# Kernel tuning notes

Measured on AMD Instinct MI355X. Metric: run time of the kernel, lower is better.

## Reference

```python
import jax, jax.numpy as jnp
import numpy as np

B, T, S = 32, 64, 64
V, E, H, Hs = 32000, 512, 512, 512
D2 = 2 * Hs  # src feature dim


def setup_inputs() -> dict:
    key = jax.random.key(0)
    ks = jax.random.split(key, 26)
    n = lambda k, shape, s=0.05: (jax.random.normal(k, shape, jnp.float32) * s)
    inp = {
        'src': jax.random.normal(ks[0], (B, S, D2), jnp.float32),
        'trg': jax.random.randint(ks[1], (B, T), 0, V),
        'mask': jnp.ones((B, T), jnp.float32),
        'emb': n(ks[2], (V, E)),
        # PyTorch LSTMCell params: weight_ih [4H, E+H], weight_hh [4H, H]
        'f_Wih': n(ks[3], (4 * H, E + H)), 'f_Whh': n(ks[4], (4 * H, H)),
        'f_bih': n(ks[5], (4 * H,)), 'f_bhh': n(ks[6], (4 * H,)),
        'b_Wih': n(ks[7], (4 * H, E + H)), 'b_Whh': n(ks[8], (4 * H, H)),
        'b_bih': n(ks[9], (4 * H,)), 'b_bhh': n(ks[10], (4 * H,)),
        # attention projections: hidden -> 2*src_hidden
        'fatt_W': n(ks[11], (D2, H)), 'fatt_b': n(ks[12], (D2,)),
        'batt_W': n(ks[13], (D2, H)), 'batt_b': n(ks[14], (D2,)),
        # att_hidden linears: (H + 2*Hs) -> H
        'fah_W': n(ks[15], (H, H + D2)), 'fah_b': n(ks[16], (H,)),
        'bah_W': n(ks[17], (H, H + D2)), 'bah_b': n(ks[18], (H,)),
        # output projection 2H -> V
        'fc_W': n(ks[19], (V, 2 * H)), 'fc_b': n(ks[20], (V,)),
        'feed_init': n(ks[21], (2 * H,), 1.0),
        'hid_init': n(ks[22], (4 * H,), 1.0),
    }
    return inp


def reference(src, trg, mask, emb, f_Wih, f_Whh, f_bih, f_bhh,
              b_Wih, b_Whh, b_bih, b_bhh, fatt_W, fatt_b, batt_W, batt_b,
              fah_W, fah_b, bah_W, bah_b, fc_W, fc_b, feed_init, hid_init):
    Bn = src.shape[0]
    Hn = feed_init.shape[0] // 2
    scale = 1.0 / np.sqrt(Hn)  # key.size(-1) == trg hidden before projection

    x = emb[trg]  # [B, T, E]  (dropout p=0 -> identity)

    hhat0 = jnp.broadcast_to(feed_init, (Bn, 2 * Hn))
    f_hhat0, b_hhat0 = jnp.split(hhat0, 2, axis=1)
    hid0 = jnp.broadcast_to(hid_init, (Bn, 4 * Hn))
    f_hid, b_hid = jnp.split(hid0, 2, axis=-1)
    f_h0, f_c0 = jnp.split(f_hid, 2, axis=-1)
    b_h0, b_c0 = jnp.split(b_hid, 2, axis=-1)

    def lstm(xin, h, c, Wih, Whh, bih, bhh):
        g = xin @ Wih.T + bih + h @ Whh.T + bhh
        i, f, gg, o = jnp.split(g, 4, axis=-1)
        c = jax.nn.sigmoid(f) * c + jax.nn.sigmoid(i) * jnp.tanh(gg)
        h = jax.nn.sigmoid(o) * jnp.tanh(c)
        return h, c

    def att(h, W, b):
        k = h @ W.T + b                              # [B, 2Hs]
        w = jnp.einsum('bd,bsd->bs', k, src) * scale  # [B, S]
        p = jax.nn.softmax(w, axis=-1)
        return jnp.einsum('bs,bsd->bd', p, src)       # [B, 2Hs]

    xs = jnp.swapaxes(x, 0, 1)      # [T, B, E]
    ms = jnp.swapaxes(mask, 0, 1)   # [T, B]

    def f_step(carry, x_t):
        h, c, hhat = carry
        h, c = lstm(jnp.concatenate([x_t, hhat], -1), h, c, f_Wih, f_Whh, f_bih, f_bhh)
        ct = att(h, fatt_W, fatt_b)
        # NOTE: original uses b_att_hidden in the forward loop (faithful)
        hhat = jnp.tanh(jnp.concatenate([h, ct], -1) @ bah_W.T + bah_b)
        return (h, c, hhat), hhat

    _, f_out = jax.lax.scan(f_step, (f_h0, f_c0, f_hhat0), xs)  # [T, B, H]

    def b_step(carry, inp):
        x_t, m_t = inp
        h, c, hhat = carry
        hn, cn = lstm(jnp.concatenate([x_t, hhat], -1), h, c, b_Wih, b_Whh, b_bih, b_bhh)
        h = m_t[:, None] * hn
        c = m_t[:, None] * cn
        ct = att(h, batt_W, batt_b)
        # NOTE: original uses f_att_hidden in the backward loop (faithful)
        hhat = jnp.tanh(jnp.concatenate([h, ct], -1) @ fah_W.T + fah_b)
        return (h, c, hhat), hhat

    _, b_out = jax.lax.scan(b_step, (b_h0, b_c0, b_hhat0), (xs[::-1], ms[::-1]))

    f_out = jnp.swapaxes(f_out, 0, 1)        # [B, T, H]
    b_cheat = jnp.swapaxes(b_out, 0, 1)      # reversed-time order, as stacked in torch
    # b_outputs[:, :-2] = b_outputs_cheat[:, 2:]; last two steps zero (faithful)
    b_shift = jnp.concatenate([b_cheat[:, 2:], jnp.zeros_like(b_cheat[:, :2])], axis=1)

    logits = jnp.concatenate([f_out, b_shift], -1) @ fc_W.T + fc_b  # [B, T, V]
    return logits
```

## Files before the change

kernel.cpp:

```cpp
#include <hip/hip_runtime.h>
#include <hip/hip_bf16.h>
#include <math.h>

typedef __hip_bfloat16 bf16;
typedef __attribute__((ext_vector_type(8))) short short8b;
typedef __attribute__((ext_vector_type(8))) __bf16 bf16x8;
typedef __attribute__((ext_vector_type(4))) float f32x4;

#define SCALE_F 0.04419417382415922f

template <typename V>
static __device__ inline auto mfma_try(V a, V b, f32x4 c, int)
    -> decltype(__builtin_amdgcn_mfma_f32_16x16x32_bf16(a, b, c, 0, 0, 0)) {
  return __builtin_amdgcn_mfma_f32_16x16x32_bf16(a, b, c, 0, 0, 0);
}
template <typename V>
static __device__ inline auto mfma_try(V a, V b, f32x4 c, long)
    -> decltype(__builtin_amdgcn_mfma_f32_16x16x32_bf16(
        __builtin_bit_cast(bf16x8, a), __builtin_bit_cast(bf16x8, b), c, 0, 0, 0)) {
  return __builtin_amdgcn_mfma_f32_16x16x32_bf16(
      __builtin_bit_cast(bf16x8, a), __builtin_bit_cast(bf16x8, b), c, 0, 0, 0);
}
static __device__ inline f32x4 MFMA(short8b a, short8b b, f32x4 c) {
  return mfma_try(a, b, c, 0);
}

static __device__ inline short8b ldb8(const bf16* p) {
  return *reinterpret_cast<const short8b*>(p);
}
static __device__ inline float b2f(bf16 v) { return __bfloat162float(v); }
static __device__ inline bf16 f2b(float v) { return __float2bfloat16(v); }
static __device__ inline float s2f(short s) {
  unsigned u = ((unsigned)(unsigned short)s) << 16;
  return __builtin_bit_cast(float, u);
}
static __device__ inline unsigned pack2(float lo, float hi) {
  const unsigned a = (unsigned)__builtin_bit_cast(unsigned short, f2b(lo));
  const unsigned b = (unsigned)__builtin_bit_cast(unsigned short, f2b(hi));
  return a | (b << 16);
}
static __device__ inline float sigm(float x) { return 1.f / (1.f + expf(-x)); }

static __device__ inline void st2_wt(bf16* p, float v) {
  unsigned ud = (unsigned)__builtin_bit_cast(unsigned short, f2b(v));
  asm volatile("global_store_short %0, %1, off sc0 sc1" ::"v"(p), "v"(ud)
               : "memory");
}
static __device__ inline void st4_wt(bf16* p, float lo, float hi) {
  unsigned ud = pack2(lo, hi);
  asm volatile("global_store_dword %0, %1, off sc0 sc1" ::"v"(p), "v"(ud)
               : "memory");
}

static __device__ inline void st_flag(unsigned* p, unsigned v) {
  asm volatile("global_store_dword %0, %1, off sc0 sc1" ::"v"(p), "v"(v)
               : "memory");
}
static __device__ inline unsigned ld_flag(const unsigned* p) {
  unsigned v;
  asm volatile("global_load_dword %0, %1, off sc0 sc1\n\ts_waitcnt vmcnt(0)"
               : "=v"(v)
               : "v"(p)
               : "memory");
  return v;
}

static __device__ inline void gbar(unsigned* flags, unsigned ep, int blk, int tid) {
  asm volatile("s_waitcnt vmcnt(0)" ::: "memory");
  __syncthreads();
  if (tid < 64) {
    unsigned* row = flags + (size_t)ep * 64;
    if (tid == 0) st_flag(row + blk, 1u);
    while (true) {
      const unsigned v = ld_flag(row + tid);
      if (__ballot(v != 0) == ~0ull) break;
      __builtin_amdgcn_s_sleep(1);
    }
  }
  __syncthreads();
}

template <typename OutT, bool HAS_BIAS>
__global__ __launch_bounds__(256) void gemm_k(
    const bf16* __restrict__ A, const bf16* __restrict__ Bw,
    OutT* __restrict__ C, const float* __restrict__ bias,
    int M, int N, int K) {
  const int lane = threadIdx.x & 63;
  const int wid = threadIdx.x >> 6;
  const int m0 = blockIdx.y * 128 + (wid >> 1) * 64;
  const int n0 = blockIdx.x * 128 + (wid & 1) * 64;
  const int lr = lane & 15;
  const int lk = (lane >> 4) * 8;
  f32x4 acc[4][4];
#pragma unroll
  for (int i = 0; i < 4; ++i)
#pragma unroll
    for (int j = 0; j < 4; ++j) acc[i][j] = (f32x4){0.f, 0.f, 0.f, 0.f};
  const bf16* Ap = A + (size_t)(m0 + lr) * K + lk;
  const bf16* Bp = Bw + (size_t)(n0 + lr) * K + lk;
  for (int k0 = 0; k0 < K; k0 += 32) {
    short8b av[4], bv[4];
#pragma unroll
    for (int i = 0; i < 4; ++i) av[i] = ldb8(Ap + (size_t)i * 16 * K + k0);
#pragma unroll
    for (int i = 0; i < 4; ++i) bv[i] = ldb8(Bp + (size_t)i * 16 * K + k0);
#pragma unroll
    for (int mi = 0; mi < 4; ++mi)
#pragma unroll
      for (int ni = 0; ni < 4; ++ni)
        acc[mi][ni] = MFMA(av[mi], bv[ni], acc[mi][ni]);
  }
  const int rb = (lane >> 4) * 4;
#pragma unroll
  for (int mi = 0; mi < 4; ++mi) {
#pragma unroll
    for (int r = 0; r < 4; ++r) {
      const int row = m0 + mi * 16 + rb + r;
#pragma unroll
      for (int ni = 0; ni < 4; ++ni) {
        const int col = n0 + ni * 16 + lr;
        float v = acc[mi][ni][r];
        if (HAS_BIAS) v += bias[col];
        if constexpr (sizeof(OutT) == 2) {
          C[(size_t)row * N + col] = f2b(v);
        } else {
          C[(size_t)row * N + col] = v;
        }
      }
    }
  }
}

__global__ void k_xg(const float* __restrict__ emb, const int* __restrict__ trg,
                     bf16* __restrict__ xg) {
  const int i = blockIdx.x * 256 + threadIdx.x;
  const int r = i >> 9, e = i & 511;
  const int t = r >> 5, b = r & 31;
  const int tok = trg[b * 64 + t];
  xg[i] = f2b(emb[(size_t)tok * 512 + e]);
}

__global__ void k_srcb(const float* __restrict__ s, bf16* __restrict__ d) {
  const int i = blockIdx.x * 256 + threadIdx.x;
  d[i] = f2b(s[i]);
}

__global__ void k_fcw(const float* __restrict__ s, bf16* __restrict__ d) {
  const size_t stride = (size_t)gridDim.x * blockDim.x;
  for (size_t i = blockIdx.x * (size_t)blockDim.x + threadIdx.x;
       i < (size_t)32000 * 1024; i += stride)
    d[i] = f2b(s[i]);
}

__global__ void k_bmt(const bf16* __restrict__ in, bf16* __restrict__ out) {
  const int i = blockIdx.x * 256 + threadIdx.x;
  const int b = i >> 15, rem = i & 32767, o = rem >> 6, s = rem & 63;
  out[i] = in[(size_t)(b * 64 + s) * 512 + o];
}

__global__ void k_wpack(const float* __restrict__ fWih, const float* __restrict__ fWhh,
                        const float* __restrict__ bWih, const float* __restrict__ bWhh,
                        const float* __restrict__ fattW, const float* __restrict__ battW,
                        const float* __restrict__ bahW, const float* __restrict__ fahW,
                        bf16* Wxf, bf16* Wxb, bf16* Wrecf, bf16* Wrecb,
                        bf16* attWtf, bf16* attWtb, bf16* ahW2f, bf16* ahW2b,
                        bf16* Wh1f, bf16* Wh1b) {
  const int stride = gridDim.x * blockDim.x;
  const int i0 = blockIdx.x * blockDim.x + threadIdx.x;
  for (int i = i0; i < 2048 * 512; i += stride) {
    const int gc = i >> 9, k = i & 511;
    Wxf[i] = f2b(fWih[(size_t)gc * 1024 + k]);
    Wxb[i] = f2b(bWih[(size_t)gc * 1024 + k]);
  }
  for (int i = i0; i < 2048 * 1024; i += stride) {
    const int gc = i >> 10, k = i & 1023;
    float vf, vb;
    if (k < 512) { vf = fWih[(size_t)gc * 1024 + 512 + k]; vb = bWih[(size_t)gc * 1024 + 512 + k]; }
    else         { vf = fWhh[(size_t)gc * 512 + k - 512]; vb = bWhh[(size_t)gc * 512 + k - 512]; }
    Wrecf[i] = f2b(vf); Wrecb[i] = f2b(vb);
  }
  for (int i = i0; i < 512 * 1024; i += stride) {
    const int j = i >> 10, d = i & 1023;
    attWtf[i] = f2b(fattW[(size_t)d * 512 + j]);
    attWtb[i] = f2b(battW[(size_t)d * 512 + j]);
  }
  for (int i = i0; i < 512 * 1024; i += stride) {
    const int o = i >> 10, d = i & 1023;
    ahW2f[i] = f2b(bahW[(size_t)o * 1536 + 512 + d]);
    ahW2b[i] = f2b(fahW[(size_t)o * 1536 + 512 + d]);
  }
  for (int i = i0; i < 512 * 512; i += stride) {
    const int o = i >> 9, k = i & 511;
    Wh1f[i] = f2b(bahW[(size_t)o * 1536 + k]);
    Wh1b[i] = f2b(fahW[(size_t)o * 1536 + k]);
  }
}

__global__ void k_c0(const float* __restrict__ src, const float* __restrict__ fb,
                     const float* __restrict__ bb, float* __restrict__ c0f,
                     float* __restrict__ c0b) {
  const int r = blockIdx.x;
  const int tid = threadIdx.x;
  float pf = 0.f, pb = 0.f;
  for (int d = tid; d < 1024; d += 256) {
    const float s = src[(size_t)r * 1024 + d];
    pf += s * fb[d];
    pb += s * bb[d];
  }
#pragma unroll
  for (int d = 1; d < 64; d <<= 1) { pf += __shfl_xor(pf, d); pb += __shfl_xor(pb, d); }
  __shared__ float rf[4], rb2[4];
  if ((tid & 63) == 0) { rf[tid >> 6] = pf; rb2[tid >> 6] = pb; }
  __syncthreads();
  if (tid == 0) {
    c0f[r] = (rf[0] + rf[1] + rf[2] + rf[3]) * SCALE_F;
    c0b[r] = (rb2[0] + rb2[1] + rb2[2] + rb2[3]) * SCALE_F;
  }
}

__global__ void k_init(const float* __restrict__ feed, const float* __restrict__ hid,
                       bf16* hh0, bf16* hh1, bf16* hb0, bf16* hb1,
                       float* cst0, float* cst1) {
  const int i = blockIdx.x * 256 + threadIdx.x;
  const int b = i >> 9, k = i & 511;
  hh0[i] = f2b(feed[k]);
  hh1[i] = f2b(feed[512 + k]);
  hb0[i] = f2b(hid[k]);
  hb1[i] = f2b(hid[1024 + k]);
  cst0[k * 32 + b] = hid[512 + k];
  cst1[k * 32 + b] = hid[1536 + k];
}

struct ScanP {
  const bf16* Wrec[2]; const bf16* Xp[2]; const bf16* Af[2]; const bf16* Bmt[2];
  const bf16* Wh1[2]; const float* bih[2]; const float* bhh[2];
  const float* c0[2]; const float* ahb[2]; const float* mask;
  bf16* hh[2]; bf16* hb[2]; bf16* U[2]; float* cst[2]; bf16* hcat; unsigned* flags;
};

__global__ __launch_bounds__(256) void scan_k(ScanP P) {
  const int blk = blockIdx.x;
  const int dir = blk >> 5;
  const int g = blk & 31;
  const int tid = threadIdx.x;
  const int lane = tid & 63;
  const int wv = tid >> 6;

  const bf16* __restrict__ Wrec = P.Wrec[dir];
  const bf16* __restrict__ Xp = P.Xp[dir];
  const bf16* __restrict__ Af = P.Af[dir];
  const bf16* __restrict__ Bmt = P.Bmt[dir];
  const bf16* __restrict__ Wh1 = P.Wh1[dir];
  const float* __restrict__ bihp = P.bih[dir];
  const float* __restrict__ bhhp = P.bhh[dir];
  const float* __restrict__ c0v = P.c0[dir];
  const float* __restrict__ ahbp = P.ahb[dir];
  bf16* __restrict__ hhB = P.hh[dir];
  bf16* __restrict__ hbB = P.hb[dir];
  bf16* __restrict__ Ubuf = P.U[dir];
  float* __restrict__ cst = P.cst[dir];

  __shared__ float gl[4][16][33];
  __shared__ float h_lds[512];
  __shared__ float w_part[2][64];
  __shared__ float p_lds[64];

  unsigned ep = 0;
  const int lr16 = lane & 15;
  const int kb = lane >> 4;
  const int koff = kb * 8;

  short8b pA0[16], pA1[16];
  {
    const bf16* A0 = hbB + (size_t)lr16 * 512;
    const bf16* A1 = hbB + (size_t)(lr16 + 16) * 512;
#pragma unroll
    for (int ks = 0; ks < 16; ++ks) {
      pA0[ks] = ldb8(A0 + ks * 32 + koff);
      pA1[ks] = ldb8(A1 + ks * 32 + koff);
    }
  }

  for (int t = 0; t < 64; ++t) {
    const bf16* hhR = hhB + (size_t)t * 32 * 512;
    bf16* hhW = hhB + (size_t)(t + 1) * 32 * 512;
    bf16* hbW = hbB + (size_t)(t + 1) * 32 * 512;

    {
      const int gate = wv;
      const int gc = gate * 512 + g * 16 + lr16;
      const bf16* Brow = Wrec + (size_t)gc * 1024;
      const bf16* A0h = hhR + (size_t)lr16 * 512;
      const bf16* A1h = hhR + (size_t)(lr16 + 16) * 512;
      f32x4 ac0 = (f32x4){0.f, 0.f, 0.f, 0.f};
      f32x4 ac1 = (f32x4){0.f, 0.f, 0.f, 0.f};
#pragma unroll
      for (int ks = 0; ks < 16; ++ks) {
        const int k = ks * 32 + koff;
        const short8b bv = ldb8(Brow + 512 + k);
        ac0 = MFMA(pA0[ks], bv, ac0);
        ac1 = MFMA(pA1[ks], bv, ac1);
      }
#pragma unroll
      for (int c = 0; c < 2; ++c) {
        short8b sa[8], sb[8];
#pragma unroll
        for (int i = 0; i < 8; ++i) {
          const int k = (c * 8 + i) * 32 + koff;
          sa[i] = ldb8(A0h + k);
          sb[i] = ldb8(A1h + k);
        }
#pragma unroll
        for (int i = 0; i < 8; ++i) {
          const int k = (c * 8 + i) * 32 + koff;
          const short8b bv = ldb8(Brow + k);
          ac0 = MFMA(sa[i], bv, ac0);
          ac1 = MFMA(sb[i], bv, ac1);
        }
      }
      const int tcol = dir ? (63 - t) : t;
      const float bsum = bihp[gc] + bhhp[gc];
      const bf16* xpc = Xp + (size_t)gc * 2048 + tcol * 32;
#pragma unroll
      for (int r = 0; r < 4; ++r) {
        const int brow = kb * 4 + r;
        gl[gate][lr16][brow] = ac0[r] + b2f(xpc[brow]) + bsum;
        gl[gate][lr16][brow + 16] = ac1[r] + b2f(xpc[brow + 16]) + bsum;
      }
    }
    __syncthreads();
    {
      const int b = tid & 31;
      const int jp = (tid >> 5) * 2;
      float hn2[2];
#pragma unroll
      for (int u = 0; u < 2; ++u) {
        const int jl = jp + u;
        const int j = g * 16 + jl;
        const float gi = gl[0][jl][b];
        const float gf = gl[1][jl][b];
        const float gg = gl[2][jl][b];
        const float go = gl[3][jl][b];
        float cn = sigm(gf) * cst[j * 32 + b] + sigm(gi) * tanhf(gg);
        float hn = sigm(go) * tanhf(cn);
        if (dir) {
          const float m = P.mask[b * 64 + (63 - t)];
          hn *= m; cn *= m;
        }
        cst[j * 32 + b] = cn;
        hn2[u] = hn;
      }
      st4_wt(hbW + (size_t)b * 512 + g * 16 + jp, hn2[0], hn2[1]);
    }
    gbar(P.flags, ep++, blk, tid);

    if (wv == 0) {
      const bf16* Brow = Wh1 + (size_t)(g * 16 + lr16) * 512;
      const bf16* A0 = hbW + (size_t)lr16 * 512;
      const bf16* A1 = hbW + (size_t)(lr16 + 16) * 512;
      f32x4 u0 = (f32x4){0.f, 0.f, 0.f, 0.f};
      f32x4 u1 = (f32x4){0.f, 0.f, 0.f, 0.f};
#pragma unroll
      for (int ks = 0; ks < 16; ++ks) {
        const int k = ks * 32 + koff;
        const short8b bv = ldb8(Brow + k);
        u0 = MFMA(ldb8(A0 + k), bv, u0);
        u1 = MFMA(ldb8(A1 + k), bv, u1);
      }
      bf16* Uw = Ubuf + (size_t)t * 32 * 512;
      const int o = g * 16 + lr16;
#pragma unroll
      for (int r = 0; r < 4; ++r) {
        const int b0 = kb * 4 + r;
        st2_wt(Uw + (size_t)b0 * 512 + o, u0[r]);
        st2_wt(Uw + (size_t)(b0 + 16) * 512 + o, u1[r]);
      }
    } else if (wv == 1) {
      const short8b v = ldb8(hbW + (size_t)g * 512 + lane * 8);
#pragma unroll
      for (int e = 0; e < 8; ++e) h_lds[lane * 8 + e] = s2f(v[e]);
    }
    __syncthreads();
    if (wv == 1 || wv == 2) {
      const int q = wv - 1;
      const bf16* arow = Af + (size_t)(g * 64 + lane) * 512 + q * 256;
      float part = 0.f;
#pragma unroll 8
      for (int k8 = 0; k8 < 256; k8 += 8) {
        const short8b v = ldb8(arow + k8);
#pragma unroll
        for (int e = 0; e < 8; ++e) part += h_lds[q * 256 + k8 + e] * s2f(v[e]);
      }
      w_part[q][lane] = part;
    }
    __syncthreads();
    if (wv == 3) {
      const float v = (w_part[0][lane] + w_part[1][lane]) * SCALE_F + c0v[g * 64 + lane];
      float mx = v;
#pragma unroll
      for (int d = 1; d < 64; d <<= 1) mx = fmaxf(mx, __shfl_xor(mx, d));
      const float e = expf(v - mx);
      float sm = e;
#pragma unroll
      for (int d = 1; d < 64; d <<= 1) sm += __shfl_xor(sm, d);
      p_lds[lane] = e / sm;
    }
    __syncthreads();
    float a2[2];
    {
      const int o2 = tid * 2;
      const bf16* bm0 = Bmt + ((size_t)g * 512 + o2) * 64;
      short8b v0[8], v1[8];
#pragma unroll
      for (int i = 0; i < 8; ++i) {
        v0[i] = ldb8(bm0 + i * 8);
        v1[i] = ldb8(bm0 + 64 + i * 8);
      }
      float s0 = ahbp[o2], s1 = ahbp[o2 + 1];
#pragma unroll
      for (int i = 0; i < 8; ++i)
#pragma unroll
        for (int e = 0; e < 8; ++e) {
          const float p = p_lds[i * 8 + e];
          s0 += p * s2f(v0[i][e]);
          s1 += p * s2f(v1[i][e]);
        }
      a2[0] = s0; a2[1] = s1;
    }
    gbar(P.flags, ep++, blk, tid);

    {
      const int o2 = tid * 2;
      const unsigned uu =
          *reinterpret_cast<const unsigned*>(Ubuf + ((size_t)t * 32 + g) * 512 + o2);
      const float h0 = tanhf(a2[0] + s2f((short)(uu & 0xffffu)));
      const float h1 = tanhf(a2[1] + s2f((short)(uu >> 16)));
      st4_wt(hhW + (size_t)g * 512 + o2, h0, h1);
      const unsigned hp = pack2(h0, h1);
      if (dir == 0) {
        *reinterpret_cast<unsigned*>(P.hcat + (size_t)(g * 64 + t) * 1024 + o2) = hp;
      } else if (t >= 2) {
        *reinterpret_cast<unsigned*>(P.hcat + (size_t)(g * 64 + t - 2) * 1024 + 512 + o2) = hp;
      }
      if (t < 63) {
        const bf16* A0 = hbW + (size_t)lr16 * 512;
        const bf16* A1 = hbW + (size_t)(lr16 + 16) * 512;
#pragma unroll
        for (int ks = 0; ks < 16; ++ks) {
          pA0[ks] = ldb8(A0 + ks * 32 + koff);
          pA1[ks] = ldb8(A1 + ks * 32 + koff);
        }
      }
    }
    gbar(P.flags, ep++, blk, tid);
  }
}

extern "C" void kernel_launch(void* const* d_in, const int* in_sizes, int n_in,
                              void* d_out, int out_size, void* d_ws, size_t ws_size,
                              hipStream_t stream) {
  (void)in_sizes; (void)n_in; (void)out_size; (void)ws_size;
  const float* src  = (const float*)d_in[0];
  const int*   trg  = (const int*)d_in[1];
  const float* mask = (const float*)d_in[2];
  const float* emb  = (const float*)d_in[3];
  const float* fWih = (const float*)d_in[4];
  const float* fWhh = (const float*)d_in[5];
  const float* fbih = (const float*)d_in[6];
  const float* fbhh = (const float*)d_in[7];
  const float* bWih = (const float*)d_in[8];
  const float* bWhh = (const float*)d_in[9];
  const float* bbih = (const float*)d_in[10];
  const float* bbhh = (const float*)d_in[11];
  const float* fattW = (const float*)d_in[12];
  const float* fattb = (const float*)d_in[13];
  const float* battW = (const float*)d_in[14];
  const float* battb = (const float*)d_in[15];
  const float* fahW = (const float*)d_in[16];
  const float* fahb = (const float*)d_in[17];
  const float* bahW = (const float*)d_in[18];
  const float* bahb = (const float*)d_in[19];
  const float* fcW  = (const float*)d_in[20];
  const float* fcb  = (const float*)d_in[21];
  const float* feed = (const float*)d_in[22];
  const float* hid  = (const float*)d_in[23];

  char* wsp = (char*)d_ws;
  size_t off = 0;
  auto alloc = [&](size_t bytes) -> void* {
    void* p = wsp + off;
    off += (bytes + 255) & ~(size_t)255;
    return p;
  };
  unsigned* flags = (unsigned*)alloc((size_t)192 * 64 * 4);
  bf16* hcat = (bf16*)alloc((size_t)2048 * 1024 * 2);
  const size_t zero_bytes = off;
  bf16* xg    = (bf16*)alloc((size_t)2048 * 512 * 2);
  bf16* srcb  = (bf16*)alloc((size_t)2048 * 1024 * 2);
  bf16* fcWb  = (bf16*)alloc((size_t)32000 * 1024 * 2);
  bf16* Wxf   = (bf16*)alloc((size_t)2048 * 512 * 2);
  bf16* Wxb   = (bf16*)alloc((size_t)2048 * 512 * 2);
  bf16* Wrecf = (bf16*)alloc((size_t)2048 * 1024 * 2);
  bf16* Wrecb = (bf16*)alloc((size_t)2048 * 1024 * 2);
  bf16* attWtf = (bf16*)alloc((size_t)512 * 1024 * 2);
  bf16* attWtb = (bf16*)alloc((size_t)512 * 1024 * 2);
  bf16* ahW2f = (bf16*)alloc((size_t)512 * 1024 * 2);
  bf16* ahW2b = (bf16*)alloc((size_t)512 * 1024 * 2);
  bf16* Wh1f  = (bf16*)alloc((size_t)512 * 512 * 2);
  bf16* Wh1b  = (bf16*)alloc((size_t)512 * 512 * 2);
  bf16* Xpf   = (bf16*)alloc((size_t)2048 * 2048 * 2);
  bf16* Xpb   = (bf16*)alloc((size_t)2048 * 2048 * 2);
  bf16* Aff   = (bf16*)alloc((size_t)2048 * 512 * 2);
  bf16* Afb   = (bf16*)alloc((size_t)2048 * 512 * 2);
  bf16* Bmf   = (bf16*)alloc((size_t)2048 * 512 * 2);
  bf16* Bmb   = (bf16*)alloc((size_t)2048 * 512 * 2);
  bf16* Bmtf  = (bf16*)alloc((size_t)2048 * 512 * 2);
  bf16* Bmtb  = (bf16*)alloc((size_t)2048 * 512 * 2);
  float* c0f  = (float*)alloc(2048 * 4);
  float* c0b  = (float*)alloc(2048 * 4);
  bf16* hh0   = (bf16*)alloc((size_t)65 * 32 * 512 * 2);
  bf16* hh1   = (bf16*)alloc((size_t)65 * 32 * 512 * 2);
  bf16* hb0   = (bf16*)alloc((size_t)65 * 32 * 512 * 2);
  bf16* hb1   = (bf16*)alloc((size_t)65 * 32 * 512 * 2);
  bf16* Uf    = (bf16*)alloc((size_t)64 * 32 * 512 * 2);
  bf16* Ub    = (bf16*)alloc((size_t)64 * 32 * 512 * 2);
  float* cst0 = (float*)alloc((size_t)512 * 32 * 4);
  float* cst1 = (float*)alloc((size_t)512 * 32 * 4);

  hipMemsetAsync(d_ws, 0, zero_bytes, stream);

  k_xg<<<4096, 256, 0, stream>>>(emb, trg, xg);
  k_srcb<<<8192, 256, 0, stream>>>(src, srcb);
  k_fcw<<<8192, 256, 0, stream>>>(fcW, fcWb);
  k_wpack<<<2048, 256, 0, stream>>>(fWih, fWhh, bWih, bWhh, fattW, battW, bahW, fahW,
                                    Wxf, Wxb, Wrecf, Wrecb, attWtf, attWtb, ahW2f, ahW2b,
                                    Wh1f, Wh1b);
  k_c0<<<2048, 256, 0, stream>>>(src, fattb, battb, c0f, c0b);
  k_init<<<64, 256, 0, stream>>>(feed, hid, hh0, hh1, hb0, hb1, cst0, cst1);

  gemm_k<bf16, false><<<dim3(16, 16), 256, 0, stream>>>(Wxf, xg, Xpf, nullptr, 2048, 2048, 512);
  gemm_k<bf16, false><<<dim3(16, 16), 256, 0, stream>>>(Wxb, xg, Xpb, nullptr, 2048, 2048, 512);
  gemm_k<bf16, false><<<dim3(4, 16), 256, 0, stream>>>(srcb, attWtf, Aff, nullptr, 2048, 512, 1024);
  gemm_k<bf16, false><<<dim3(4, 16), 256, 0, stream>>>(srcb, attWtb, Afb, nullptr, 2048, 512, 1024);
  gemm_k<bf16, false><<<dim3(4, 16), 256, 0, stream>>>(srcb, ahW2f, Bmf, nullptr, 2048, 512, 1024);
  gemm_k<bf16, false><<<dim3(4, 16), 256, 0, stream>>>(srcb, ahW2b, Bmb, nullptr, 2048, 512, 1024);
  k_bmt<<<4096, 256, 0, stream>>>(Bmf, Bmtf);
  k_bmt<<<4096, 256, 0, stream>>>(Bmb, Bmtb);

  ScanP sp;
  sp.Wrec[0] = Wrecf; sp.Wrec[1] = Wrecb;
  sp.Xp[0] = Xpf;     sp.Xp[1] = Xpb;
  sp.Af[0] = Aff;     sp.Af[1] = Afb;
  sp.Bmt[0] = Bmtf;   sp.Bmt[1] = Bmtb;
  sp.Wh1[0] = Wh1f;   sp.Wh1[1] = Wh1b;
  sp.bih[0] = fbih;   sp.bih[1] = bbih;
  sp.bhh[0] = fbhh;   sp.bhh[1] = bbhh;
  sp.c0[0] = c0f;     sp.c0[1] = c0b;
  sp.ahb[0] = bahb;   sp.ahb[1] = fahb;
  sp.mask = mask;
  sp.hh[0] = hh0;     sp.hh[1] = hh1;
  sp.hb[0] = hb0;     sp.hb[1] = hb1;
  sp.U[0] = Uf;       sp.U[1] = Ub;
  sp.cst[0] = cst0;   sp.cst[1] = cst1;
  sp.hcat = hcat;     sp.flags = flags;
  scan_k<<<64, 256, 0, stream>>>(sp);

  gemm_k<float, true><<<dim3(250, 16), 256, 0, stream>>>(hcat, fcWb, (float*)d_out, fcb,
                                                         2048, 32000, 1024);
}
```

Baseline: 2.867 ms.

## Fuse input projection into scan and add LDS-tiled output GEMM

Drops the two precomputed input-projection GEMMs and their 2048x2048 intermediate buffers. The scan kernel now computes the x_t @ Wx contribution with extra MFMAs each step, reading embeddings and input weights directly. Separately, the final vocabulary projection moves to a new kernel that stages 128x128 tiles in shared memory and prefetches the next K slice into registers, and it launches on a 1D grid ordered M-fastest. The fusion adds work inside the latency-bound serial scan, which may lengthen each step.

```diff
diff --git a/kernel.cpp b/kernel.cpp
--- a/kernel.cpp
+++ b/kernel.cpp
@@ -126,6 +126,69 @@
         } else {
           C[(size_t)row * N + col] = v;
         }
+      }
+    }
+  }
+}
+
+__global__ __launch_bounds__(256) void gemm_out(
+    const bf16* __restrict__ A, const bf16* __restrict__ Bw,
+    float* __restrict__ C, const float* __restrict__ bias) {
+  constexpr int K = 1024, N = 32000;
+  __shared__ bf16 As[128 * 32];
+  __shared__ bf16 Bs[128 * 32];
+  const int wgid = blockIdx.x;
+  const int mt = wgid & 15, nt = wgid >> 4;
+  const int tid = threadIdx.x, lane = tid & 63, wv = tid >> 6;
+  const int m0 = mt * 128, n0 = nt * 128;
+  const int lr16 = lane & 15, kb = lane >> 4, koff = kb * 8;
+  const int r0 = tid >> 2, q0 = tid & 3;
+  const int r1 = (tid + 256) >> 2;
+  const bf16* Ap0 = A + (size_t)(m0 + r0) * K + q0 * 8;
+  const bf16* Ap1 = A + (size_t)(m0 + r1) * K + q0 * 8;
+  const bf16* Bp0 = Bw + (size_t)(n0 + r0) * K + q0 * 8;
+  const bf16* Bp1 = Bw + (size_t)(n0 + r1) * K + q0 * 8;
+  const int wm = (wv >> 1) * 64, wn = (wv & 1) * 64;
+  f32x4 acc[4][4];
+#pragma unroll
+  for (int i = 0; i < 4; ++i)
+#pragma unroll
+    for (int j = 0; j < 4; ++j) acc[i][j] = (f32x4){0.f, 0.f, 0.f, 0.f};
+  short8b a0 = ldb8(Ap0), a1 = ldb8(Ap1), b0 = ldb8(Bp0), b1 = ldb8(Bp1);
+  for (int k0 = 0; k0 < K; k0 += 32) {
+    __syncthreads();
+    *reinterpret_cast<short8b*>(&As[tid * 8]) = a0;
+    *reinterpret_cast<short8b*>(&As[(tid + 256) * 8]) = a1;
+    *reinterpret_cast<short8b*>(&Bs[tid * 8]) = b0;
+    *reinterpret_cast<short8b*>(&Bs[(tid + 256) * 8]) = b1;
+    __syncthreads();
+    if (k0 + 32 < K) {
+      a0 = ldb8(Ap0 + k0 + 32);
+      a1 = ldb8(Ap1 + k0 + 32);
+      b0 = ldb8(Bp0 + k0 + 32);
+      b1 = ldb8(Bp1 + k0 + 32);
+    }
+    short8b af[4], bfr[4];
+#pragma unroll
+    for (int i = 0; i < 4; ++i) {
+      af[i] = *reinterpret_cast<const short8b*>(&As[(wm + i * 16 + lr16) * 32 + koff]);
+      bfr[i] = *reinterpret_cast<const short8b*>(&Bs[(wn + i * 16 + lr16) * 32 + koff]);
+    }
+#pragma unroll
+    for (int mi = 0; mi < 4; ++mi)
+#pragma unroll
+      for (int ni = 0; ni < 4; ++ni)
+        acc[mi][ni] = MFMA(af[mi], bfr[ni], acc[mi][ni]);
+  }
+#pragma unroll
+  for (int mi = 0; mi < 4; ++mi) {
+#pragma unroll
+    for (int r = 0; r < 4; ++r) {
+      const int row = m0 + wm + mi * 16 + kb * 4 + r;
+#pragma unroll
+      for (int ni = 0; ni < 4; ++ni) {
+        const int col = n0 + wn + ni * 16 + lr16;
+        C[(size_t)row * N + col] = acc[mi][ni][r] + bias[col];
       }
     }
   }
@@ -232,8 +295,9 @@
 }
 
 struct ScanP {
-  const bf16* Wrec[2]; const bf16* Xp[2]; const bf16* Af[2]; const bf16* Bmt[2];
-  const bf16* Wh1[2]; const float* bih[2]; const float* bhh[2];
+  const bf16* Wrec[2]; const bf16* Wx[2]; const bf16* xg;
+  const bf16* Af[2]; const bf16* Bmt[2]; const bf16* Wh1[2];
+  const float* bih[2]; const float* bhh[2];
   const float* c0[2]; const float* ahb[2]; const float* mask;
   bf16* hh[2]; bf16* hb[2]; bf16* U[2]; float* cst[2]; bf16* hcat; unsigned* flags;
 };
@@ -247,7 +311,8 @@
   const int wv = tid >> 6;
 
   const bf16* __restrict__ Wrec = P.Wrec[dir];
-  const bf16* __restrict__ Xp = P.Xp[dir];
+  const bf16* __restrict__ Wx = P.Wx[dir];
+  const bf16* __restrict__ xg = P.xg;
   const bf16* __restrict__ Af = P.Af[dir];
   const bf16* __restrict__ Bmt = P.Bmt[dir];
   const bf16* __restrict__ Wh1 = P.Wh1[dir];
@@ -289,9 +354,13 @@
     {
       const int gate = wv;
       const int gc = gate * 512 + g * 16 + lr16;
+      const int tcol = dir ? (63 - t) : t;
       const bf16* Brow = Wrec + (size_t)gc * 1024;
+      const bf16* Bxrow = Wx + (size_t)gc * 512;
       const bf16* A0h = hhR + (size_t)lr16 * 512;
       const bf16* A1h = hhR + (size_t)(lr16 + 16) * 512;
+      const bf16* A0x = xg + ((size_t)tcol * 32 + lr16) * 512;
+      const bf16* A1x = A0x + (size_t)16 * 512;
       f32x4 ac0 = (f32x4){0.f, 0.f, 0.f, 0.f};
       f32x4 ac1 = (f32x4){0.f, 0.f, 0.f, 0.f};
 #pragma unroll
@@ -318,14 +387,29 @@
           ac1 = MFMA(sb[i], bv, ac1);
         }
       }
-      const int tcol = dir ? (63 - t) : t;
+#pragma unroll
+      for (int c = 0; c < 2; ++c) {
+        short8b sa[8], sb[8];
+#pragma unroll
+        for (int i = 0; i < 8; ++i) {
+          const int k = (c * 8 + i) * 32 + koff;
+          sa[i] = ldb8(A0x + k);
+          sb[i] = ldb8(A1x + k);
+        }
+#pragma unroll
+        for (int i = 0; i < 8; ++i) {
+          const int k = (c * 8 + i) * 32 + koff;
+          const short8b bv = ldb8(Bxrow + k);
+          ac0 = MFMA(sa[i], bv, ac0);
+          ac1 = MFMA(sb[i], bv, ac1);
+        }
+      }
       const float bsum = bihp[gc] + bhhp[gc];
-      const bf16* xpc = Xp + (size_t)gc * 2048 + tcol * 32;
 #pragma unroll
       for (int r = 0; r < 4; ++r) {
         const int brow = kb * 4 + r;
-        gl[gate][lr16][brow] = ac0[r] + b2f(xpc[brow]) + bsum;
-        gl[gate][lr16][brow + 16] = ac1[r] + b2f(xpc[brow + 16]) + bsum;
+        gl[gate][lr16][brow] = ac0[r] + bsum;
+        gl[gate][lr16][brow + 16] = ac1[r] + bsum;
       }
     }
     __syncthreads();
@@ -508,8 +592,6 @@
   bf16* ahW2b = (bf16*)alloc((size_t)512 * 1024 * 2);
   bf16* Wh1f  = (bf16*)alloc((size_t)512 * 512 * 2);
   bf16* Wh1b  = (bf16*)alloc((size_t)512 * 512 * 2);
-  bf16* Xpf   = (bf16*)alloc((size_t)2048 * 2048 * 2);
-  bf16* Xpb   = (bf16*)alloc((size_t)2048 * 2048 * 2);
   bf16* Aff   = (bf16*)alloc((size_t)2048 * 512 * 2);
   bf16* Afb   = (bf16*)alloc((size_t)2048 * 512 * 2);
   bf16* Bmf   = (bf16*)alloc((size_t)2048 * 512 * 2);
@@ -538,8 +620,6 @@
   k_c0<<<2048, 256, 0, stream>>>(src, fattb, battb, c0f, c0b);
   k_init<<<64, 256, 0, stream>>>(feed, hid, hh0, hh1, hb0, hb1, cst0, cst1);
 
-  gemm_k<bf16, false><<<dim3(16, 16), 256, 0, stream>>>(Wxf, xg, Xpf, nullptr, 2048, 2048, 512);
-  gemm_k<bf16, false><<<dim3(16, 16), 256, 0, stream>>>(Wxb, xg, Xpb, nullptr, 2048, 2048, 512);
   gemm_k<bf16, false><<<dim3(4, 16), 256, 0, stream>>>(srcb, attWtf, Aff, nullptr, 2048, 512, 1024);
   gemm_k<bf16, false><<<dim3(4, 16), 256, 0, stream>>>(srcb, attWtb, Afb, nullptr, 2048, 512, 1024);
   gemm_k<bf16, false><<<dim3(4, 16), 256, 0, stream>>>(srcb, ahW2f, Bmf, nullptr, 2048, 512, 1024);
@@ -549,7 +629,8 @@
 
   ScanP sp;
   sp.Wrec[0] = Wrecf; sp.Wrec[1] = Wrecb;
-  sp.Xp[0] = Xpf;     sp.Xp[1] = Xpb;
+  sp.Wx[0] = Wxf;     sp.Wx[1] = Wxb;
+  sp.xg = xg;
   sp.Af[0] = Aff;     sp.Af[1] = Afb;
   sp.Bmt[0] = Bmtf;   sp.Bmt[1] = Bmtb;
   sp.Wh1[0] = Wh1f;   sp.Wh1[1] = Wh1b;
@@ -565,6 +646,5 @@
   sp.hcat = hcat;     sp.flags = flags;
   scan_k<<<64, 256, 0, stream>>>(sp);
 
-  gemm_k<float, true><<<dim3(250, 16), 256, 0, stream>>>(hcat, fcWb, (float*)d_out, fcb,
-                                                         2048, 32000, 1024);
-}
+  gemm_out<<<4000, 256, 0, stream>>>(hcat, fcWb, (float*)d_out, fcb);
+}
```

Result: slower. 2.941 ms (+2.6%).
